# Performance work log

Hardware: AMD Instinct MI355X
Metric: run time of the kernel (lower is better)

## Reference

```python
import jax, jax.numpy as jnp
import numpy as np

WS = 8   # window_size
SS = 4   # shift_size
NH = 4   # num_heads


def _window_partition(x, w):
    B, H, W, C = x.shape
    x = x.reshape(B, H // w, w, W // w, w, C).transpose(0, 1, 3, 2, 4, 5)
    return x.reshape(-1, w, w, C)


def _window_reverse(win, w, H, W):
    B = win.shape[0] // ((H // w) * (W // w))
    x = win.reshape(B, H // w, W // w, w, w, -1).transpose(0, 1, 3, 2, 4, 5)
    return x.reshape(B, H, W, -1)


def _rel_pos_index(w):
    coords = np.stack(np.meshgrid(np.arange(w), np.arange(w), indexing='ij'))  # (2,w,w)
    cf = coords.reshape(2, -1)
    rel = cf[:, :, None] - cf[:, None, :]          # (2,N,N)
    rel = rel.transpose(1, 2, 0)                   # (N,N,2)
    rel[:, :, 0] += w - 1
    rel[:, :, 1] += w - 1
    rel[:, :, 0] *= 2 * w - 1
    return rel.sum(-1)                             # (N,N) int


def _attn_mask(Hp, Wp, w, ss):
    if ss == 0:
        return None
    img = np.zeros((1, Hp, Wp, 1), np.float32)
    slices = (slice(0, -w), slice(-w, -ss), slice(-ss, None))
    cnt = 0
    for h in slices:
        for ww in slices:
            img[:, h, ww, :] = cnt
            cnt += 1
    mw = img.reshape(1, Hp // w, w, Wp // w, w, 1).transpose(0, 1, 3, 2, 4, 5).reshape(-1, w * w)
    m = mw[:, None, :] - mw[:, :, None]
    return np.where(m != 0, -100.0, 0.0).astype(np.float32)  # (nW,N,N)


def _ln(x, g, b, eps=1e-5):
    mu = x.mean(-1, keepdims=True)
    var = ((x - mu) ** 2).mean(-1, keepdims=True)
    return (x - mu) * jax.lax.rsqrt(var + eps) * g + b


def setup_inputs() -> dict:
    key = jax.random.key(0)
    ks = jax.random.split(key, 8)
    B, H, W, C = 4, 256, 256, 128
    hid = 4 * C
    s = 0.02
    return {
        'x': jax.random.normal(ks[0], (B, H * W, C), jnp.float32),
        'norm1_g': jnp.ones((C,), jnp.float32),
        'norm1_b': jnp.zeros((C,), jnp.float32),
        'qkv_w': jax.random.normal(ks[1], (3 * C, C), jnp.float32) * s,
        'qkv_b': jnp.zeros((3 * C,), jnp.float32),
        'rpb_table': jax.random.normal(ks[2], ((2 * WS - 1) ** 2, NH), jnp.float32) * s,
        'proj_w': jax.random.normal(ks[3], (C, C), jnp.float32) * s,
        'proj_b': jnp.zeros((C,), jnp.float32),
        'norm2_g': jnp.ones((C,), jnp.float32),
        'norm2_b': jnp.zeros((C,), jnp.float32),
        'fc1_w': jax.random.normal(ks[4], (hid, C), jnp.float32) * s,
        'fc1_b': jnp.zeros((hid,), jnp.float32),
        'fc2_w': jax.random.normal(ks[5], (C, hid), jnp.float32) * s,
        'fc2_b': jnp.zeros((C,), jnp.float32),
        'H': H,
        'W': W,
    }


def reference(x, norm1_g, norm1_b, qkv_w, qkv_b, rpb_table, proj_w, proj_b,
              norm2_g, norm2_b, fc1_w, fc1_b, fc2_w, fc2_b, H, W):
    B, L, C = x.shape
    hd = C // NH
    scale = hd ** -0.5
    N = WS * WS

    shortcut = x
    h = _ln(x, norm1_g, norm1_b).reshape(B, H, W, C)

    pad_r = (WS - W % WS) % WS
    pad_b = (WS - H % WS) % WS
    if pad_r > 0 or pad_b > 0:
        h = jnp.pad(h, ((0, 0), (0, pad_b), (0, pad_r), (0, 0)))
    Hp, Wp = H + pad_b, W + pad_r

    if SS > 0:
        h = jnp.roll(h, (-SS, -SS), axis=(1, 2))

    win = _window_partition(h, WS).reshape(-1, N, C)   # (B_,N,C)
    B_ = win.shape[0]

    qkv = (win @ qkv_w.T + qkv_b).reshape(B_, N, 3, NH, hd).transpose(2, 0, 3, 1, 4)
    q, k, v = qkv[0] * scale, qkv[1], qkv[2]           # (B_,NH,N,hd)

    attn = jnp.einsum('whnd,whmd->whnm', q, k)         # (B_,NH,N,N)
    rpi = _rel_pos_index(WS).reshape(-1)
    bias = rpb_table[rpi].reshape(N, N, NH).transpose(2, 0, 1)
    attn = attn + bias[None]

    mask = _attn_mask(Hp, Wp, WS, SS)
    if mask is not None:
        nW = mask.shape[0]
        attn = attn.reshape(B_ // nW, nW, NH, N, N) + jnp.asarray(mask)[None, :, None]
        attn = attn.reshape(B_, NH, N, N)

    attn = jax.nn.softmax(attn, axis=-1)
    out = jnp.einsum('whnm,whmd->whnd', attn, v).transpose(0, 2, 1, 3).reshape(B_, N, C)
    out = out @ proj_w.T + proj_b

    out = _window_reverse(out.reshape(-1, WS, WS, C), WS, Hp, Wp)
    if SS > 0:
        out = jnp.roll(out, (SS, SS), axis=(1, 2))
    if pad_r > 0 or pad_b > 0:
        out = out[:, :H, :W, :]
    x = shortcut + out.reshape(B, H * W, C)

    y = _ln(x, norm2_g, norm2_b)
    y = jax.nn.gelu(y @ fc1_w.T + fc1_b, approximate=False) @ fc2_w.T + fc2_b
    return x + y
```

## Files before the change

### kernel.cpp

```cpp
#include <hip/hip_runtime.h>
#include <hip/hip_bf16.h>

typedef unsigned short u16;
typedef unsigned int u32;
typedef __attribute__((ext_vector_type(8))) short bf16x8;
typedef __attribute__((ext_vector_type(4))) float f32x4;

__device__ __forceinline__ u32 fbits(float f) { union { float f; u32 u; } a; a.f = f; return a.u; }
__device__ __forceinline__ u16 f2bf(float f) {
    u32 u = fbits(f);
    return (u16)((u + 0x7FFFu + ((u >> 16) & 1u)) >> 16);
}
__device__ __forceinline__ u16 bfr(float f) { return (u16)((fbits(f) + 0x8000u) >> 16); }
__device__ __forceinline__ u32 pk2(float lo, float hi) {
    return __builtin_amdgcn_perm(fbits(hi) + 0x8000u, fbits(lo) + 0x8000u, 0x07060302u);
}
__device__ __forceinline__ float bf2f(u16 b) {
    union { u32 u; float f; } a; a.u = ((u32)b) << 16; return a.f;
}
__device__ __forceinline__ float gelu_poly(float t) {
    float u = fminf(3.0f, fmaxf(-3.0f, t));
    float u2 = u * u;
    float w = fmaf(u2, 0.00319581f, -0.0550159f);
    w = fmaf(u2, w, 0.401174f);
    float sg = fmaf(u, w, 0.5f);
    return t * sg;
}

#define MFMA(a, b, c) __builtin_amdgcn_mfma_f32_16x16x32_bf16(a, b, c, 0, 0, 0)

__device__ __forceinline__ void gload16(const u16* g, u16* l) {
    __builtin_amdgcn_global_load_lds(
        (const __attribute__((address_space(1))) void*)g,
        (__attribute__((address_space(3))) void*)l, 16, 0, 0);
}

__global__ void swin_prep_kernel(const float* __restrict__ qkv_w, const float* __restrict__ proj_w,
                                 const float* __restrict__ fc1_w, const float* __restrict__ fc2_w,
                                 const float* __restrict__ rpb, u16* __restrict__ wout,
                                 float* __restrict__ bias_lane)
{
    int idx = blockIdx.x * 256 + threadIdx.x;
    if (idx < 49152) wout[idx] = f2bf(qkv_w[idx]);
    else if (idx < 81920) {
        int j = idx - 49152;
        int tile = j >> 9, lane = (j >> 3) & 63, e = j & 7;
        int nt = tile >> 2, ks = tile & 3;
        wout[idx] = f2bf(proj_w[(nt * 16 + (lane & 15)) * 128 + ks * 32 + (lane >> 4) * 8 + e]);
    } else if (idx < 212992) {
        int j = idx - 81920;
        int chunk = j >> 13, rest = j & 8191;
        int tile = rest >> 9, lane = (rest >> 3) & 63, e = rest & 7;
        int lg = lane >> 4;
        float v;
        if (tile < 8) {
            int mh = tile >> 2, ks = tile & 3;
            v = fc1_w[(chunk * 32 + mh * 16 + (lane & 15)) * 128 + ks * 32 + lg * 8 + e];
        } else {
            int nt = tile - 8;
            int hid = (e < 4) ? (lg * 4 + e) : (16 + lg * 4 + (e - 4));
            v = fc2_w[(nt * 16 + (lane & 15)) * 512 + chunk * 32 + hid];
        }
        wout[idx] = f2bf(v);
    } else {
        int t = idx - 212992;
        int r = t & 3, lane = (t >> 2) & 63, nt = (t >> 8) & 3, mt = (t >> 10) & 3;
        int h = (t >> 12) & 3, v = (t >> 14) & 3;
        int i = mt * 16 + ((lane >> 4) << 2) + r;
        int j = nt * 16 + (lane & 15);
        int ri = i >> 3, ci = i & 7, rj = j >> 3, cj = j & 7;
        int rpi = (ri - rj + 7) * 15 + (ci - cj + 7);
        float bv = rpb[rpi * 4 + h];
        int vh = v >> 1, vw = v & 1;
        int regi = (vh ? (ri < 4 ? 1 : 2) : 0) * 3 + (vw ? (ci < 4 ? 1 : 2) : 0);
        int regj = (vh ? (rj < 4 ? 1 : 2) : 0) * 3 + (vw ? (cj < 4 ? 1 : 2) : 0);
        if (regi != regj) bv -= 100.0f;
        bias_lane[t] = bv * 1.4426950408889634f;
    }
}

__global__ __launch_bounds__(512, 4) void swin_attn_kernel(
    const float* __restrict__ x, const float* __restrict__ g1, const float* __restrict__ b1,
    const float* __restrict__ qkvb, const u16* __restrict__ qkvw,
    const float* __restrict__ bias_lane, u16* __restrict__ attn_out)
{
    __shared__ __align__(16) u16 ldsX[8448];
    __shared__ __align__(16) u16 ldsQK[17408];
    __shared__ float sb[640];

    int tid = threadIdx.x;
    int wid = blockIdx.x;
    int bb_ = wid >> 10, wh = (wid >> 5) & 31, ww = wid & 31;

    for (int i = tid; i < 640; i += 512) {
        float v;
        if (i < 128) v = g1[i];
        else if (i < 256) v = b1[i - 128];
        else v = qkvb[i - 256];
        sb[i] = v;
    }

    int trow = tid >> 3, seg = tid & 7;
    int rn = trow >> 3, cn = trow & 7;
    int srow = (wh * 8 + rn + 4) & 255;
    int scol = (ww * 8 + cn + 4) & 255;
    long grow = (long)bb_ * 65536 + srow * 256 + scol;
    const float4* xrow = (const float4*)(x + grow * 128 + seg * 16);
    float4 xv[4];
    #pragma unroll
    for (int i = 0; i < 4; ++i) xv[i] = xrow[i];
    __syncthreads();

    float s1 = 0.0f, s2 = 0.0f;
    #pragma unroll
    for (int i = 0; i < 4; ++i) {
        float4 v = xv[i];
        s1 += v.x + v.y + v.z + v.w;
        s2 += v.x * v.x + v.y * v.y + v.z * v.z + v.w * v.w;
    }
    #pragma unroll
    for (int off = 1; off < 8; off <<= 1) { s1 += __shfl_xor(s1, off); s2 += __shfl_xor(s2, off); }
    float mu = s1 * 0.0078125f;
    float rstd = rsqrtf(s2 * 0.0078125f - mu * mu + 1e-5f);
    {
        u32 pk[8];
        #pragma unroll
        for (int i = 0; i < 4; ++i) {
            float vv[4] = {xv[i].x, xv[i].y, xv[i].z, xv[i].w};
            float y0, y1, y2, y3;
            {
                int c = seg * 16 + i * 4;
                y0 = (vv[0] - mu) * rstd * sb[c + 0] + sb[128 + c + 0];
                y1 = (vv[1] - mu) * rstd * sb[c + 1] + sb[128 + c + 1];
                y2 = (vv[2] - mu) * rstd * sb[c + 2] + sb[128 + c + 2];
                y3 = (vv[3] - mu) * rstd * sb[c + 3] + sb[128 + c + 3];
            }
            pk[i * 2]     = pk2(y0, y1);
            pk[i * 2 + 1] = pk2(y2, y3);
        }
        *(uint4*)&ldsX[trow * 132 + seg * 16] = *(uint4*)&pk[0];
        *(uint4*)&ldsX[trow * 132 + seg * 16 + 8] = *(uint4*)&pk[4];
    }
    __syncthreads();

    int wave = tid >> 6, lane = tid & 63, l15 = lane & 15, lg = lane >> 4;
    int mrow = lg * 4;
    bf16x8 afr[4][4];
    #pragma unroll
    for (int mt = 0; mt < 4; ++mt)
        #pragma unroll
        for (int ks = 0; ks < 4; ++ks)
            afr[mt][ks] = *(const bf16x8*)&ldsX[(mt * 16 + l15) * 132 + ks * 32 + lg * 8];
    __syncthreads();
    #pragma unroll 1
    for (int nn = 0; nn < 3; ++nn) {
        int nt = wave * 3 + nn;
        int n = nt * 16 + l15;
        const u16* wp = qkvw + n * 128 + lg * 8;
        bf16x8 bfr_[4];
        #pragma unroll
        for (int ks = 0; ks < 4; ++ks) bfr_[ks] = *(const bf16x8*)(wp + ks * 32);
        f32x4 acc[4];
        #pragma unroll
        for (int mt = 0; mt < 4; ++mt) acc[mt] = (f32x4){0.0f, 0.0f, 0.0f, 0.0f};
        #pragma unroll
        for (int ks = 0; ks < 4; ++ks)
            #pragma unroll
            for (int mt = 0; mt < 4; ++mt)
                acc[mt] = MFMA(afr[mt][ks], bfr_[ks], acc[mt]);
        float bias = sb[256 + n];
        if (n < 128) {
            #pragma unroll
            for (int mt = 0; mt < 4; ++mt)
                #pragma unroll
                for (int r = 0; r < 4; ++r)
                    ldsQK[(mt * 16 + mrow + r) * 132 + n] = bfr(acc[mt][r] + bias);
        } else if (n < 256) {
            #pragma unroll
            for (int mt = 0; mt < 4; ++mt)
                #pragma unroll
                for (int r = 0; r < 4; ++r)
                    ldsQK[8448 + (mt * 16 + mrow + r) * 132 + (n - 128)] = bfr(acc[mt][r] + bias);
        } else {
            int row = n - 256;
            int sw = (row & 7) << 4;
            #pragma unroll
            for (int mt = 0; mt < 4; ++mt) {
                uint2 pv;
                pv.x = pk2(acc[mt][0] + bias, acc[mt][1] + bias);
                pv.y = pk2(acc[mt][2] + bias, acc[mt][3] + bias);
                int cb = ((mt * 16 + mrow) * 2) ^ sw;
                *(uint2*)((char*)ldsX + row * 128 + cb) = pv;
            }
        }
    }
    __syncthreads();

    int h = wave >> 1, half = wave & 1;
    int v4 = ((wh == 31) ? 2 : 0) | ((ww == 31) ? 1 : 0);
    const float4* blp = (const float4*)bias_lane;
    bf16x8 bk[4];
    #pragma unroll
    for (int nt = 0; nt < 4; ++nt)
        bk[nt] = *(const bf16x8*)&ldsQK[8448 + (nt * 16 + l15) * 132 + h * 32 + lg * 8];
    f32x4 sS[2][4];
    #pragma unroll
    for (int m2 = 0; m2 < 2; ++m2) {
        int mt = half * 2 + m2;
        bf16x8 aq = *(const bf16x8*)&ldsQK[(mt * 16 + l15) * 132 + h * 32 + lg * 8];
        #pragma unroll
        for (int nt = 0; nt < 4; ++nt) {
            f32x4 z = (f32x4){0.0f, 0.0f, 0.0f, 0.0f};
            z = MFMA(aq, bk[nt], z);
            float4 bl = blp[((v4 * 4 + h) * 16 + mt * 4 + nt) * 64 + lane];
            sS[m2][nt][0] = z[0] * 0.2550349f + bl.x;
            sS[m2][nt][1] = z[1] * 0.2550349f + bl.y;
            sS[m2][nt][2] = z[2] * 0.2550349f + bl.z;
            sS[m2][nt][3] = z[3] * 0.2550349f + bl.w;
        }
    }
    float rinv[2][4];
    #pragma unroll
    for (int m2 = 0; m2 < 2; ++m2) {
        #pragma unroll
        for (int r = 0; r < 4; ++r) {
            float sum = 0.0f;
            #pragma unroll
            for (int nt = 0; nt < 4; ++nt) {
                float p = exp2f(sS[m2][nt][r]);
                sS[m2][nt][r] = p;
                sum += p;
            }
            #pragma unroll
            for (int off = 1; off < 16; off <<= 1) sum += __shfl_xor(sum, off);
            rinv[m2][r] = __builtin_amdgcn_rcpf(sum);
        }
    }
    __syncthreads();
    #pragma unroll
    for (int m2 = 0; m2 < 2; ++m2) {
        int mt = half * 2 + m2;
        #pragma unroll
        for (int nt = 0; nt < 4; ++nt)
            #pragma unroll
            for (int r = 0; r < 4; ++r)
                ldsQK[h * 4352 + (mt * 16 + mrow + r) * 68 + nt * 16 + l15] = bfr(sS[m2][nt][r]);
    }
    __syncthreads();

    f32x4 o[2][2];
    #pragma unroll
    for (int m2 = 0; m2 < 2; ++m2)
        #pragma unroll
        for (int np = 0; np < 2; ++np) o[m2][np] = (f32x4){0.0f, 0.0f, 0.0f, 0.0f};
    #pragma unroll
    for (int kt = 0; kt < 2; ++kt) {
        bf16x8 pa[2];
        #pragma unroll
        for (int m2 = 0; m2 < 2; ++m2) {
            int mt = half * 2 + m2;
            pa[m2] = *(const bf16x8*)&ldsQK[h * 4352 + (mt * 16 + l15) * 68 + kt * 32 + lg * 8];
        }
        #pragma unroll
        for (int np = 0; np < 2; ++np) {
            int vr = h * 32 + np * 16 + l15;
            int cb = (kt * 64 + lg * 16) ^ ((vr & 7) << 4);
            bf16x8 bv = *(const bf16x8*)((const char*)ldsX + vr * 128 + cb);
            #pragma unroll
            for (int m2 = 0; m2 < 2; ++m2)
                o[m2][np] = MFMA(pa[m2], bv, o[m2][np]);
        }
    }
    __syncthreads();
    #pragma unroll
    for (int m2 = 0; m2 < 2; ++m2) {
        int mt = half * 2 + m2;
        #pragma unroll
        for (int np = 0; np < 2; ++np)
            #pragma unroll
            for (int r = 0; r < 4; ++r)
                ldsX[(mt * 16 + mrow + r) * 132 + h * 32 + np * 16 + l15] = bfr(o[m2][np][r] * rinv[m2][r]);
    }
    __syncthreads();
    u16* op = attn_out + grow * 128 + seg * 16;
    *(uint4*)op = *(const uint4*)&ldsX[trow * 132 + seg * 16];
    *(uint4*)(op + 8) = *(const uint4*)&ldsX[trow * 132 + seg * 16 + 8];
}

__global__ __launch_bounds__(256, 3) void swin_mlp_kernel(
    const u16* __restrict__ attn, const float* __restrict__ x,
    const u16* __restrict__ projws, const u16* __restrict__ wms,
    const float* __restrict__ projb, const float* __restrict__ g2, const float* __restrict__ b2,
    const float* __restrict__ f1b, const float* __restrict__ f2b, float* __restrict__ out)
{
    __shared__ __align__(16) u16 wbuf[2][8192];
    __shared__ __align__(16) u16 sbuf[4][576];

    int tid = threadIdx.x;
    int wave = tid >> 6, lane = tid & 63, l15 = lane & 15, lg = lane >> 4;
    long wbase = (long)blockIdx.x * 128 + wave * 32;

    {
        const u16* src = wms + wave * 2048 + lane * 8;
        u16* dst = &wbuf[0][wave * 2048];
        #pragma unroll
        for (int i = 0; i < 4; ++i)
            gload16(src + i * 512, dst + i * 512);
    }

    const u16* arow = attn + (wbase + l15) * 128 + lg * 8;
    bf16x8 aat[2][4];
    #pragma unroll
    for (int ks = 0; ks < 4; ++ks) {
        aat[0][ks] = *(const bf16x8*)(arow + ks * 32);
        aat[1][ks] = *(const bf16x8*)(arow + 2048 + ks * 32);
    }

    f32x4 pacc[2][8];
    #pragma unroll
    for (int nt = 0; nt < 8; ++nt) {
        const u16* wp = projws + nt * 2048 + lane * 8;
        pacc[0][nt] = (f32x4){0.0f, 0.0f, 0.0f, 0.0f};
        pacc[1][nt] = (f32x4){0.0f, 0.0f, 0.0f, 0.0f};
        #pragma unroll
        for (int ks = 0; ks < 4; ++ks) {
            bf16x8 bw = *(const bf16x8*)(wp + ks * 512);
            pacc[0][nt] = MFMA(aat[0][ks], bw, pacc[0][nt]);
            pacc[1][nt] = MFMA(aat[1][ks], bw, pacc[1][nt]);
        }
    }

    #pragma unroll
    for (int nt = 0; nt < 8; ++nt) {
        float pb = projb[nt * 16 + l15];
        #pragma unroll
        for (int mt = 0; mt < 2; ++mt)
            #pragma unroll
            for (int r = 0; r < 4; ++r)
                pacc[mt][nt][r] += x[(wbase + mt * 16 + lg * 4 + r) * 128 + nt * 16 + l15] + pb;
    }
    float mu[2][4], rstd[2][4];
    #pragma unroll
    for (int mt = 0; mt < 2; ++mt)
        #pragma unroll
        for (int r = 0; r < 4; ++r) {
            float a = 0.0f, bq = 0.0f;
            #pragma unroll
            for (int nt = 0; nt < 8; ++nt) { a += pacc[mt][nt][r]; bq += pacc[mt][nt][r] * pacc[mt][nt][r]; }
            #pragma unroll
            for (int off = 1; off < 16; off <<= 1) { a += __shfl_xor(a, off); bq += __shfl_xor(bq, off); }
            mu[mt][r] = a * 0.0078125f;
            rstd[mt][r] = rsqrtf(bq * 0.0078125f - mu[mt][r] * mu[mt][r] + 1e-5f);
        }
    u16* hb = (u16*)sbuf[wave];
    bf16x8 ay[2][4];
    #pragma unroll
    for (int p = 0; p < 4; ++p) {
        #pragma unroll
        for (int mt = 0; mt < 2; ++mt) {
            #pragma unroll
            for (int n2 = 0; n2 < 2; ++n2) {
                int c = p * 32 + n2 * 16 + l15;
                float gg = g2[c], bb = b2[c];
                int nt = p * 2 + n2;
                #pragma unroll
                for (int r = 0; r < 4; ++r)
                    hb[(lg * 4 + r) * 36 + n2 * 16 + l15] =
                        bfr((pacc[mt][nt][r] - mu[mt][r]) * rstd[mt][r] * gg + bb);
            }
            __builtin_amdgcn_sched_barrier(0);
            ay[mt][p] = *(const bf16x8*)&hb[l15 * 36 + lg * 8];
            __builtin_amdgcn_sched_barrier(0);
        }
    }
    #pragma unroll
    for (int nt = 0; nt < 8; ++nt) {
        float fb = f2b[nt * 16 + l15];
        #pragma unroll
        for (int mt = 0; mt < 2; ++mt)
            #pragma unroll
            for (int r = 0; r < 4; ++r)
                pacc[mt][nt][r] += fb;
    }
    __syncthreads();

    #pragma unroll 1
    for (int cc = 0; cc < 16; ++cc) {
        int cur = cc & 1;
        if (cc < 15) {
            const u16* src = wms + (cc + 1) * 8192 + wave * 2048 + lane * 8;
            u16* dst = &wbuf[cur ^ 1][wave * 2048];
            #pragma unroll
            for (int i = 0; i < 4; ++i)
                gload16(src + i * 512, dst + i * 512);
        }
        f32x4 h[2][2];
        h[0][0] = h[0][1] = h[1][0] = h[1][1] = (f32x4){0.0f, 0.0f, 0.0f, 0.0f};
        #pragma unroll
        for (int mh = 0; mh < 2; ++mh)
            #pragma unroll
            for (int ks = 0; ks < 4; ++ks) {
                bf16x8 w1 = *(const bf16x8*)&wbuf[cur][(mh * 4 + ks) * 512 + lane * 8];
                h[0][mh] = MFMA(w1, ay[0][ks], h[0][mh]);
                h[1][mh] = MFMA(w1, ay[1][ks], h[1][mh]);
            }
        float4 fb0 = *(const float4*)(f1b + cc * 32 + lg * 4);
        float4 fb1 = *(const float4*)(f1b + cc * 32 + 16 + lg * 4);
        float b0[4] = {fb0.x, fb0.y, fb0.z, fb0.w};
        float b1[4] = {fb1.x, fb1.y, fb1.z, fb1.w};
        bf16x8 ah[2];
        #pragma unroll
        for (int mt = 0; mt < 2; ++mt) {
            float g0[4], g1[4];
            #pragma unroll
            for (int r = 0; r < 4; ++r) {
                g0[r] = gelu_poly(h[mt][0][r] + b0[r]);
                g1[r] = gelu_poly(h[mt][1][r] + b1[r]);
            }
            union { u32 w[4]; bf16x8 v; } u_;
            u_.w[0] = pk2(g0[0], g0[1]);
            u_.w[1] = pk2(g0[2], g0[3]);
            u_.w[2] = pk2(g1[0], g1[1]);
            u_.w[3] = pk2(g1[2], g1[3]);
            ah[mt] = u_.v;
        }
        #pragma unroll
        for (int nt = 0; nt < 8; ++nt) {
            bf16x8 bw = *(const bf16x8*)&wbuf[cur][(8 + nt) * 512 + lane * 8];
            pacc[0][nt] = MFMA(ah[0], bw, pacc[0][nt]);
            pacc[1][nt] = MFMA(ah[1], bw, pacc[1][nt]);
        }
        __syncthreads();
    }
    #pragma unroll
    for (int nt = 0; nt < 8; ++nt)
        #pragma unroll
        for (int mt = 0; mt < 2; ++mt)
            #pragma unroll
            for (int r = 0; r < 4; ++r)
                out[(wbase + mt * 16 + lg * 4 + r) * 128 + nt * 16 + l15] = pacc[mt][nt][r];
}

extern "C" void kernel_launch(void* const* d_in, const int* in_sizes, int n_in,
                              void* d_out, int out_size, void* d_ws, size_t ws_size,
                              hipStream_t stream)
{
    const float* x     = (const float*)d_in[0];
    const float* n1g   = (const float*)d_in[1];
    const float* n1b   = (const float*)d_in[2];
    const float* qkvw  = (const float*)d_in[3];
    const float* qkvb  = (const float*)d_in[4];
    const float* rpb   = (const float*)d_in[5];
    const float* projw = (const float*)d_in[6];
    const float* projb = (const float*)d_in[7];
    const float* n2g   = (const float*)d_in[8];
    const float* n2b   = (const float*)d_in[9];
    const float* f1w   = (const float*)d_in[10];
    const float* f1b   = (const float*)d_in[11];
    const float* f2w   = (const float*)d_in[12];
    const float* f2b   = (const float*)d_in[13];

    char* ws = (char*)d_ws;
    u16* attn_buf = (u16*)ws;
    u16* wb = (u16*)(ws + 67108864);
    float* bias_lane = (float*)(ws + 67108864 + 425984);
    u16* qkvwb  = wb;
    u16* projws = wb + 49152;
    u16* wms    = wb + 81920;

    swin_prep_kernel<<<1088, 256, 0, stream>>>(qkvw, projw, f1w, f2w, rpb, wb, bias_lane);
    swin_attn_kernel<<<4096, 512, 0, stream>>>(x, n1g, n1b, qkvb, qkvwb, bias_lane, attn_buf);
    swin_mlp_kernel<<<2048, 256, 0, stream>>>(attn_buf, x, projws, wms,
                                              projb, n2g, n2b, f1b, f2b, (float*)d_out);
}
```

Before: 235.1 us.

## Keep softmax probabilities in registers by computing transposed QK^T scores

Swaps the MFMA operands so each lane holds score values along the key dimension in the layout the PV MFMA needs as its A operand. The probabilities are packed to bf16 in registers and fed directly to the PV MFMA, removing the LDS round trip of the P matrix and two block barriers. The bias table layout and the V storage swizzle are permuted to match. Row sums now need only two cross-lane shuffles, but normalisation needs per-element shuffles to fetch each row's reciprocal in the output stage.

```diff
diff --git a/kernel.cpp b/kernel.cpp
--- a/kernel.cpp
+++ b/kernel.cpp
@@ -66,8 +66,8 @@
         int t = idx - 212992;
         int r = t & 3, lane = (t >> 2) & 63, nt = (t >> 8) & 3, mt = (t >> 10) & 3;
         int h = (t >> 12) & 3, v = (t >> 14) & 3;
-        int i = mt * 16 + ((lane >> 4) << 2) + r;
-        int j = nt * 16 + (lane & 15);
+        int i = mt * 16 + (lane & 15);
+        int j = nt * 16 + ((lane >> 4) << 2) + r;
         int ri = i >> 3, ci = i & 7, rj = j >> 3, cj = j & 7;
         int rpi = (ri - rj + 7) * 15 + (ci - cj + 7);
         float bv = rpb[rpi * 4 + h];
@@ -85,7 +85,7 @@
     const float* __restrict__ bias_lane, u16* __restrict__ attn_out)
 {
     __shared__ __align__(16) u16 ldsX[8448];
-    __shared__ __align__(16) u16 ldsQK[17408];
+    __shared__ __align__(16) u16 ldsQK[16896];
     __shared__ float sb[640];
 
     int tid = threadIdx.x;
@@ -189,7 +189,7 @@
                 uint2 pv;
                 pv.x = pk2(acc[mt][0] + bias, acc[mt][1] + bias);
                 pv.y = pk2(acc[mt][2] + bias, acc[mt][3] + bias);
-                int cb = ((mt * 16 + mrow) * 2) ^ sw;
+                int cb = ((mt >> 1) * 64 + mrow * 4 + (mt & 1) * 8) ^ sw;
                 *(uint2*)((char*)ldsX + row * 128 + cb) = pv;
             }
         }
@@ -203,15 +203,18 @@
     #pragma unroll
     for (int nt = 0; nt < 4; ++nt)
         bk[nt] = *(const bf16x8*)&ldsQK[8448 + (nt * 16 + l15) * 132 + h * 32 + lg * 8];
+    bf16x8 aq[2];
+    #pragma unroll
+    for (int m2 = 0; m2 < 2; ++m2)
+        aq[m2] = *(const bf16x8*)&ldsQK[((half * 2 + m2) * 16 + l15) * 132 + h * 32 + lg * 8];
     f32x4 sS[2][4];
     #pragma unroll
     for (int m2 = 0; m2 < 2; ++m2) {
         int mt = half * 2 + m2;
-        bf16x8 aq = *(const bf16x8*)&ldsQK[(mt * 16 + l15) * 132 + h * 32 + lg * 8];
         #pragma unroll
         for (int nt = 0; nt < 4; ++nt) {
             f32x4 z = (f32x4){0.0f, 0.0f, 0.0f, 0.0f};
-            z = MFMA(aq, bk[nt], z);
+            z = MFMA(bk[nt], aq[m2], z);
             float4 bl = blp[((v4 * 4 + h) * 16 + mt * 4 + nt) * 64 + lane];
             sS[m2][nt][0] = z[0] * 0.2550349f + bl.x;
             sS[m2][nt][1] = z[1] * 0.2550349f + bl.y;
@@ -219,35 +222,22 @@
             sS[m2][nt][3] = z[3] * 0.2550349f + bl.w;
         }
     }
-    float rinv[2][4];
+    float rinv[2];
     #pragma unroll
     for (int m2 = 0; m2 < 2; ++m2) {
-        #pragma unroll
-        for (int r = 0; r < 4; ++r) {
-            float sum = 0.0f;
-            #pragma unroll
-            for (int nt = 0; nt < 4; ++nt) {
+        float sum = 0.0f;
+        #pragma unroll
+        for (int nt = 0; nt < 4; ++nt)
+            #pragma unroll
+            for (int r = 0; r < 4; ++r) {
                 float p = exp2f(sS[m2][nt][r]);
                 sS[m2][nt][r] = p;
                 sum += p;
             }
-            #pragma unroll
-            for (int off = 1; off < 16; off <<= 1) sum += __shfl_xor(sum, off);
-            rinv[m2][r] = __builtin_amdgcn_rcpf(sum);
-        }
-    }
-    __syncthreads();
-    #pragma unroll
-    for (int m2 = 0; m2 < 2; ++m2) {
-        int mt = half * 2 + m2;
-        #pragma unroll
-        for (int nt = 0; nt < 4; ++nt)
-            #pragma unroll
-            for (int r = 0; r < 4; ++r)
-                ldsQK[h * 4352 + (mt * 16 + mrow + r) * 68 + nt * 16 + l15] = bfr(sS[m2][nt][r]);
-    }
-    __syncthreads();
-
+        sum += __shfl_xor(sum, 16);
+        sum += __shfl_xor(sum, 32);
+        rinv[m2] = __builtin_amdgcn_rcpf(sum);
+    }
     f32x4 o[2][2];
     #pragma unroll
     for (int m2 = 0; m2 < 2; ++m2)
@@ -258,8 +248,12 @@
         bf16x8 pa[2];
         #pragma unroll
         for (int m2 = 0; m2 < 2; ++m2) {
-            int mt = half * 2 + m2;
-            pa[m2] = *(const bf16x8*)&ldsQK[h * 4352 + (mt * 16 + l15) * 68 + kt * 32 + lg * 8];
+            union { u32 w[4]; bf16x8 v; } u_;
+            u_.w[0] = pk2(sS[m2][2 * kt][0], sS[m2][2 * kt][1]);
+            u_.w[1] = pk2(sS[m2][2 * kt][2], sS[m2][2 * kt][3]);
+            u_.w[2] = pk2(sS[m2][2 * kt + 1][0], sS[m2][2 * kt + 1][1]);
+            u_.w[3] = pk2(sS[m2][2 * kt + 1][2], sS[m2][2 * kt + 1][3]);
+            pa[m2] = u_.v;
         }
         #pragma unroll
         for (int np = 0; np < 2; ++np) {
@@ -278,8 +272,10 @@
         #pragma unroll
         for (int np = 0; np < 2; ++np)
             #pragma unroll
-            for (int r = 0; r < 4; ++r)
-                ldsX[(mt * 16 + mrow + r) * 132 + h * 32 + np * 16 + l15] = bfr(o[m2][np][r] * rinv[m2][r]);
+            for (int r = 0; r < 4; ++r) {
+                float rq = __shfl(rinv[m2], lg * 4 + r);
+                ldsX[(mt * 16 + mrow + r) * 132 + h * 32 + np * 16 + l15] = bfr(o[m2][np][r] * rq);
+            }
     }
     __syncthreads();
     u16* op = attn_out + grow * 128 + seg * 16;
```

New measurement: 230.6 us. About the same (-1.9%).
